# Performance work log

Measured on AMD Instinct MI355X. Metric: run time of the kernel, lower is better.

Reference implementation:

```python
import jax, jax.numpy as jnp
import numpy as np

N, E, NG = 4096, 8192, 256
AF, BF, H, L = 9, 4, 128, 3
LN_EPS = 1e-5


def _layernorm(x, g, b):
    mu = jnp.mean(x, axis=-1, keepdims=True)
    var = jnp.var(x, axis=-1, keepdims=True)
    return (x - mu) * jax.lax.rsqrt(var + LN_EPS) * g + b


def setup_inputs() -> dict:
    key = jax.random.key(0)
    ks = jax.random.split(key, 20)
    x = jax.random.normal(ks[0], (N, AF), dtype=jnp.float32)
    edge_index = jax.random.randint(ks[1], (2, E), 0, N, dtype=jnp.int64)
    edge_attr = jax.random.normal(ks[2], (E, BF), dtype=jnp.float32)
    batch = jnp.sort(jax.random.randint(ks[3], (N,), 0, NG, dtype=jnp.int64))
    s = lambda f: 1.0 / np.sqrt(f)
    return {
        "x": x, "edge_index": edge_index, "edge_attr": edge_attr, "batch": batch,
        "atom_w": jax.random.normal(ks[4], (AF, H), jnp.float32) * s(AF),
        "atom_b": jnp.zeros((H,), jnp.float32),
        # per-layer edge-network params, stacked over L layers
        "e1_w": jax.random.normal(ks[5], (L, BF, H), jnp.float32) * s(BF),
        "e1_b": jnp.zeros((L, H), jnp.float32),
        "e2_w": jax.random.normal(ks[6], (L, H, H * H), jnp.float32) * s(H),
        "e2_b": jnp.zeros((L, H * H), jnp.float32),
        "root_w": jax.random.normal(ks[7], (L, H, H), jnp.float32) * s(H),
        "conv_b": jnp.zeros((L, H), jnp.float32),
        "ln_g": jnp.ones((L, H), jnp.float32),
        "ln_b": jnp.zeros((L, H), jnp.float32),
        "head_w1": jax.random.normal(ks[8], (H, H // 2), jnp.float32) * s(H),
        "head_b1": jnp.zeros((H // 2,), jnp.float32),
        "head_w2": jax.random.normal(ks[9], (H // 2, 1), jnp.float32) * s(H // 2),
        "head_b2": jnp.zeros((1,), jnp.float32),
    }


def reference(x, edge_index, edge_attr, batch, atom_w, atom_b, e1_w, e1_b,
              e2_w, e2_b, root_w, conv_b, ln_g, ln_b, head_w1, head_b1,
              head_w2, head_b2):
    src, dst = edge_index[0], edge_index[1]
    h = jax.nn.relu(x @ atom_w + atom_b)  # [N, H]
    # in-degree for mean aggregation (empty -> 0 via clamp on denominator)
    deg = jax.ops.segment_sum(jnp.ones((E,), h.dtype), dst, num_segments=N)
    denom = jnp.maximum(deg, 1.0)[:, None]
    for l in range(L):
        # edge network: bond features -> per-edge HxH weight matrix
        eh = jax.nn.gelu(edge_attr @ e1_w[l] + e1_b[l], approximate=False)
        w = (eh @ e2_w[l] + e2_b[l]).reshape(E, H, H)  # [E, H, H]
        # gather source node features, per-edge matvec, scatter-mean to dst
        msg = jnp.einsum('ei,eio->eo', h[src], w)  # [E, H]
        agg = jax.ops.segment_sum(msg, dst, num_segments=N) / denom
        h_new = jax.nn.relu(agg + h @ root_w[l] + conv_b[l])
        h = _layernorm(h + h_new, ln_g[l], ln_b[l])
        # dropout: eval mode (identity)
    # global mean pool over graphs
    cnt = jnp.maximum(jax.ops.segment_sum(jnp.ones((N,), h.dtype), batch, num_segments=NG), 1.0)
    mol = jax.ops.segment_sum(h, batch, num_segments=NG) / cnt[:, None]
    hid = jax.nn.gelu(mol @ head_w1 + head_b1, approximate=False)
    logits = (hid @ head_w2 + head_b2).squeeze(-1)  # [NG]
    return logits
```

## Files before the change

### kernel.cpp

```cpp
#include <hip/hip_runtime.h>
#include <hip/hip_bf16.h>

#define N_NODES 4096
#define N_EDGES 8192
#define NGRAPH  256
#define AFEAT   9
#define BFEAT   4
#define H       128
#define NL      3
#define KS      129
#define SPLITS  4
#define TILE_E  64
#define SLICE_SH    16384
#define SLICE_BYTES 32768
#define WREG_BYTES  8192

typedef short short8 __attribute__((ext_vector_type(8)));
typedef short short4v __attribute__((ext_vector_type(4)));
typedef float f32x4 __attribute__((ext_vector_type(4)));

__device__ __forceinline__ short f2b(float f){
    union { float f; unsigned u; } c; c.f = f;
    unsigned r = c.u + 0x7FFFu + ((c.u >> 16) & 1u);
    return (short)(r >> 16);
}
__device__ __forceinline__ float b2f(short b){
    union { unsigned u; float f; } c;
    c.u = ((unsigned)(unsigned short)b) << 16;
    return c.f;
}
__device__ __forceinline__ float gelu_exact(float x){
    return 0.5f * x * (1.0f + erff(x * 0.70710678118654752440f));
}
__device__ __forceinline__ void async_copy16(const void* g, void* l){
    typedef __attribute__((address_space(1))) const char AS1C;
    typedef __attribute__((address_space(3))) char AS3;
    __builtin_amdgcn_global_load_lds((AS1C*)g, (AS3*)l, 16, 0, 0);
}

__global__ void k_prep_b(const float* __restrict__ e2w, const float* __restrict__ e2b,
                         short* __restrict__ bt){
    __shared__ float ts[H][33];
    int b  = blockIdx.x;
    int o0 = (b & 3) * 32;
    int k  = (b >> 2) % KS;
    int l  = (b >> 2) / KS;
    const float* src = (k < H) ? (e2w + ((size_t)l * H + k) * (H * H))
                               : (e2b + (size_t)l * (H * H));
    for (int idx = threadIdx.x; idx < H * 32; idx += 256){
        int i = idx >> 5, op = idx & 31;
        ts[i][op] = src[i * H + o0 + op];
    }
    __syncthreads();
    short* dst = bt + (size_t)(l * KS + k) * SLICE_SH;
    for (int idx = threadIdx.x; idx < 32 * H; idx += 256){
        int j    = idx & 7;
        int quad = (idx >> 3) & 3;
        int op   = (idx >> 5) & 31;
        int ic   = idx >> 10;
        int i    = ic * 32 + quad * 8 + j;
        int o    = o0 + op;
        dst[((((o >> 4) * 4 + ic) * 64) + quad * 16 + (o & 15)) * 8 + j] = f2b(ts[i][op]);
    }
}

__global__ void k_atom(const float* __restrict__ x, const float* __restrict__ aw,
                       const float* __restrict__ ab, float* __restrict__ h,
                       short* __restrict__ hb){
    __shared__ float xs[AFEAT];
    int n = blockIdx.x, o = threadIdx.x;
    if (o < AFEAT) xs[o] = x[n * AFEAT + o];
    __syncthreads();
    float a = ab[o];
    #pragma unroll
    for (int f = 0; f < AFEAT; ++f) a += xs[f] * aw[f * H + o];
    a = fmaxf(a, 0.0f);
    h[(size_t)n * H + o]  = a;
    hb[(size_t)n * H + o] = f2b(a);
}

__global__ void k_deg(const int* __restrict__ ei, int* __restrict__ ideg){
    int e = blockIdx.x * 256 + threadIdx.x;
    if (e < N_EDGES) atomicAdd(&ideg[ei[N_EDGES + e]], 1);
}

__global__ void k_scan(const int* __restrict__ ideg, int* __restrict__ row_ptr,
                       int* __restrict__ cursor){
    __shared__ int part[256];
    int t = threadIdx.x;
    int base = t * 16;
    int loc[16]; int s = 0;
    #pragma unroll
    for (int i = 0; i < 16; ++i){ loc[i] = s; s += ideg[base + i]; }
    part[t] = s;
    __syncthreads();
    if (t == 0){
        int run = 0;
        for (int i = 0; i < 256; ++i){ int v = part[i]; part[i] = run; run += v; }
        row_ptr[N_NODES] = run;
    }
    __syncthreads();
    int off = part[t];
    #pragma unroll
    for (int i = 0; i < 16; ++i){
        row_ptr[base + i] = off + loc[i];
        cursor[base + i]  = off + loc[i];
    }
}

__global__ void k_fill(const int* __restrict__ ei, int* __restrict__ cursor,
                       int* __restrict__ eidx){
    int e = blockIdx.x * 256 + threadIdx.x;
    if (e < N_EDGES){
        int d = ei[N_EDGES + e];
        int pos = atomicAdd(&cursor[d], 1);
        eidx[pos] = e;
    }
}

__global__ void k_edge_mlp(const float* __restrict__ ea, const float* __restrict__ w1,
                           const float* __restrict__ b1, short* __restrict__ ehT){
    __shared__ float as[BFEAT];
    int e = blockIdx.x, o = threadIdx.x;
    if (o < BFEAT) as[o] = ea[e * BFEAT + o];
    __syncthreads();
    #pragma unroll
    for (int l = 0; l < NL; ++l){
        float v = b1[l * H + o];
        #pragma unroll
        for (int f = 0; f < BFEAT; ++f) v += as[f] * w1[(l * BFEAT + f) * H + o];
        v = gelu_exact(v);
        ehT[((size_t)l * KS + o) * N_EDGES + e] = f2b(v);
        if (o == 0) ehT[((size_t)l * KS + H) * N_EDGES + e] = f2b(1.0f);
    }
}

__global__ __launch_bounds__(256, 2)
void k_msg_gemm(const short* __restrict__ bt, const short* __restrict__ ehT,
                const short* __restrict__ hb, const int* __restrict__ ei,
                float* __restrict__ parts, int l){
    __shared__ __align__(16) char smem[2 * 4 * WREG_BYTES + 33 * TILE_E * 2];
    short* ehs = (short*)(smem + 2 * 4 * WREG_BYTES);

    const int tid  = threadIdx.x;
    const int lane = tid & 63, w = tid >> 6;
    const int col  = lane & 15, quad = lane >> 4;

    const int split = blockIdx.x & 3;
    const int tile  = blockIdx.x >> 2;
    const int kbeg  = (KS * split) >> 2;
    const int kend  = (KS * (split + 1)) >> 2;
    const int kcnt  = kend - kbeg;
    const int ebase = tile * TILE_E;

    for (int idx = tid; idx < kcnt * TILE_E; idx += 256){
        int kk = idx >> 6, e = idx & 63;
        ehs[idx] = ehT[((size_t)(l * KS + kbeg + kk)) * N_EDGES + ebase + e];
    }

    short8 gf[4][4];
    #pragma unroll
    for (int m = 0; m < 4; ++m){
        int e = ebase + m * 16 + col;
        int s = ei[e];
        const char* gb = (const char*)hb + ((size_t)s * H + quad * 8) * 2;
        #pragma unroll
        for (int ic = 0; ic < 4; ++ic)
            gf[m][ic] = *(const short8*)(gb + ic * 64);
    }

    float acc[4][2][4];
    #pragma unroll
    for (int m = 0; m < 4; ++m)
        #pragma unroll
        for (int ot = 0; ot < 2; ++ot)
            #pragma unroll
            for (int r = 0; r < 4; ++r) acc[m][ot][r] = 0.0f;

    const char* bsrc = (const char*)bt + (size_t)(l * KS + kbeg) * SLICE_BYTES
                     + w * WREG_BYTES;
    char* lws = smem + w * WREG_BYTES;

    #pragma unroll
    for (int i = 0; i < 8; ++i)
        async_copy16(bsrc + i * 1024 + lane * 16, lws + i * 1024 + lane * 16);

    __syncthreads();

    for (int kk = 0; kk < kcnt; ++kk){
        if (kk + 1 < kcnt){
            const char* g = bsrc + (size_t)(kk + 1) * SLICE_BYTES;
            char* d = lws + ((kk + 1) & 1) * (4 * WREG_BYTES);
            asm volatile("s_waitcnt lgkmcnt(0)" ::: "memory");
            #pragma unroll
            for (int i = 0; i < 8; ++i)
                async_copy16(g + i * 1024 + lane * 16, d + i * 1024 + lane * 16);
            asm volatile("s_waitcnt vmcnt(8)" ::: "memory");
        } else {
            asm volatile("s_waitcnt vmcnt(0)" ::: "memory");
        }
        const char* Bl = lws + (kk & 1) * (4 * WREG_BYTES);

        short4v ev[4];
        #pragma unroll
        for (int m = 0; m < 4; ++m)
            ev[m] = *(const short4v*)(ehs + kk * TILE_E + m * 16 + quad * 4);

        __builtin_amdgcn_s_setprio(1);
        #pragma unroll
        for (int ot = 0; ot < 2; ++ot){
            short8 bf[4];
            #pragma unroll
            for (int ic = 0; ic < 4; ++ic)
                bf[ic] = *(const short8*)(Bl + (ot * 4 + ic) * 1024 + lane * 16);
            #pragma unroll
            for (int m = 0; m < 4; ++m){
                f32x4 U = {0.0f, 0.0f, 0.0f, 0.0f};
                #pragma unroll
                for (int ic = 0; ic < 4; ++ic)
                    U = __builtin_amdgcn_mfma_f32_16x16x32_bf16(gf[m][ic], bf[ic], U, 0, 0, 0);
                #pragma unroll
                for (int r = 0; r < 4; ++r)
                    acc[m][ot][r] += b2f(ev[m][r]) * U[r];
            }
        }
        __builtin_amdgcn_s_setprio(0);
    }

    float* pb = parts + (size_t)split * N_EDGES * H + (size_t)ebase * H + w * 32;
    #pragma unroll
    for (int m = 0; m < 4; ++m)
        #pragma unroll
        for (int r = 0; r < 4; ++r){
            float* row = pb + (m * 16 + quad * 4 + r) * H;
            #pragma unroll
            for (int ot = 0; ot < 2; ++ot)
                row[ot * 16 + col] = acc[m][ot][r];
        }
}

__global__ void k_node(const float* __restrict__ parts, const int* __restrict__ eidx,
                       const int* __restrict__ row_ptr,
                       const float* __restrict__ rw, const float* __restrict__ cb,
                       const float* __restrict__ lg, const float* __restrict__ lb,
                       float* __restrict__ h, short* __restrict__ hb, int l){
    __shared__ float hs[H];
    __shared__ float rsum[2], rsq[2];
    int n = blockIdx.x, o = threadIdx.x;
    float hv = h[(size_t)n * H + o];
    hs[o] = hv;
    int p0 = row_ptr[n], p1 = row_ptr[n + 1];
    float a = 0.0f;
    for (int p = p0; p < p1; ++p){
        const float* pr = parts + (size_t)eidx[p] * H + o;
        #pragma unroll
        for (int s = 0; s < SPLITS; ++s) a += pr[(size_t)s * N_EDGES * H];
    }
    int d = p1 - p0;
    a *= 1.0f / (float)(d > 0 ? d : 1);
    __syncthreads();
    float root = cb[l * H + o];
    const float* W = rw + (size_t)l * H * H;
    #pragma unroll 8
    for (int i = 0; i < H; ++i) root += hs[i] * W[i * H + o];
    float hn = fmaxf(a + root, 0.0f);
    float v  = hv + hn;
    float s = v, q = v * v;
    #pragma unroll
    for (int off = 32; off > 0; off >>= 1){
        s += __shfl_down(s, off, 64);
        q += __shfl_down(q, off, 64);
    }
    if ((o & 63) == 0){ rsum[o >> 6] = s; rsq[o >> 6] = q; }
    __syncthreads();
    float S = rsum[0] + rsum[1], Q = rsq[0] + rsq[1];
    float mean = S * (1.0f / H);
    float var  = Q * (1.0f / H) - mean * mean;
    float out  = (v - mean) * rsqrtf(var + 1e-5f) * lg[l * H + o] + lb[l * H + o];
    h[(size_t)n * H + o]  = out;
    hb[(size_t)n * H + o] = f2b(out);
}

__global__ void k_pool(const float* __restrict__ h, const int* __restrict__ batch,
                       float* __restrict__ molsum, float* __restrict__ cnt){
    int idx = blockIdx.x * 256 + threadIdx.x;
    int n = idx >> 7, o = idx & 127;
    int b = batch[n];
    atomicAdd(&molsum[b * H + o], h[idx]);
    if (o == 0) atomicAdd(&cnt[b], 1.0f);
}

__global__ void k_head(const float* __restrict__ molsum, const float* __restrict__ cnt,
                       const float* __restrict__ w1, const float* __restrict__ b1,
                       const float* __restrict__ w2, const float* __restrict__ b2,
                       float* __restrict__ out){
    __shared__ float mol[H];
    int g = blockIdx.x, t = threadIdx.x;
    float c = fmaxf(cnt[g], 1.0f);
    mol[t]      = molsum[g * H + t] / c;
    mol[t + 64] = molsum[g * H + t + 64] / c;
    __syncthreads();
    float a = b1[t];
    #pragma unroll 8
    for (int i = 0; i < H; ++i) a += mol[i] * w1[i * 64 + t];
    float hid = gelu_exact(a);
    float p = hid * w2[t];
    #pragma unroll
    for (int off = 32; off > 0; off >>= 1) p += __shfl_down(p, off, 64);
    if (t == 0) out[g] = p + b2[0];
}

extern "C" void kernel_launch(void* const* d_in, const int* in_sizes, int n_in,
                              void* d_out, int out_size, void* d_ws, size_t ws_size,
                              hipStream_t stream){
    (void)in_sizes; (void)n_in; (void)out_size; (void)ws_size;
    const float* x     = (const float*)d_in[0];
    const int*   ei    = (const int*)  d_in[1];
    const float* ea    = (const float*)d_in[2];
    const int*   batch = (const int*)  d_in[3];
    const float* aw    = (const float*)d_in[4];
    const float* ab    = (const float*)d_in[5];
    const float* e1w   = (const float*)d_in[6];
    const float* e1b   = (const float*)d_in[7];
    const float* e2w   = (const float*)d_in[8];
    const float* e2b   = (const float*)d_in[9];
    const float* rw    = (const float*)d_in[10];
    const float* cb    = (const float*)d_in[11];
    const float* lg    = (const float*)d_in[12];
    const float* lb    = (const float*)d_in[13];
    const float* hw1   = (const float*)d_in[14];
    const float* hb1   = (const float*)d_in[15];
    const float* hw2   = (const float*)d_in[16];
    const float* hb2   = (const float*)d_in[17];
    float* out = (float*)d_out;

    char* p = (char*)d_ws;
    auto carve = [&](size_t bytes){ char* r = p; p += (bytes + 255) & ~(size_t)255; return r; };
    short* bt     = (short*)carve((size_t)NL * KS * SLICE_SH * 2);
    float* h      = (float*)carve((size_t)N_NODES * H * 4);
    short* hbuf   = (short*)carve((size_t)N_NODES * H * 2);
    short* ehT    = (short*)carve((size_t)NL * KS * N_EDGES * 2);
    float* parts  = (float*)carve((size_t)SPLITS * N_EDGES * H * 4);
    int*   ideg   = (int*)  carve((size_t)N_NODES * 4);
    int*   row_ptr= (int*)  carve((size_t)(N_NODES + 1) * 4);
    int*   cursor = (int*)  carve((size_t)N_NODES * 4);
    int*   eidx   = (int*)  carve((size_t)N_EDGES * 4);
    float* molsum = (float*)carve((size_t)NGRAPH * H * 4);
    float* cnt    = (float*)carve((size_t)NGRAPH * 4);

    hipMemsetAsync(ideg, 0, (size_t)N_NODES * 4, stream);
    hipMemsetAsync(molsum, 0, (size_t)NGRAPH * H * 4, stream);
    hipMemsetAsync(cnt, 0, (size_t)NGRAPH * 4, stream);

    k_prep_b<<<NL * KS * 4, 256, 0, stream>>>(e2w, e2b, bt);
    k_atom<<<N_NODES, H, 0, stream>>>(x, aw, ab, h, hbuf);
    k_deg<<<N_EDGES / 256, 256, 0, stream>>>(ei, ideg);
    k_scan<<<1, 256, 0, stream>>>(ideg, row_ptr, cursor);
    k_fill<<<N_EDGES / 256, 256, 0, stream>>>(ei, cursor, eidx);
    k_edge_mlp<<<N_EDGES, H, 0, stream>>>(ea, e1w, e1b, ehT);

    for (int l = 0; l < NL; ++l){
        k_msg_gemm<<<(N_EDGES / TILE_E) * SPLITS, 256, 0, stream>>>(bt, ehT, hbuf, ei, parts, l);
        k_node<<<N_NODES, H, 0, stream>>>(parts, eidx, row_ptr, rw, cb, lg, lb, h, hbuf, l);
    }
    k_pool<<<N_NODES * H / 256, 256, 0, stream>>>(h, batch, molsum, cnt);
    k_head<<<NGRAPH, 64, 0, stream>>>(molsum, cnt, hw1, hb1, hw2, hb2, out);
}
```

Before: 320.1 us.

## Load message-GEMM B slices straight to registers and split output columns across blocks

Drops the async global-to-LDS double buffer for the per-edge weight slices. Each wave now loads its B fragments straight into registers with a two-slice ping-pong prefetch. The output columns are split into two halves across twice as many blocks, so each wave computes 16 columns instead of 32, which cuts register and LDS pressure and raises parallelism. The edge-MLP activations are stored as fp32 instead of bf16, removing the bf16 conversion in the inner loop. In exchange, the hidden-feature gather and ehT loads are repeated per half, and the ehT buffer is twice as large.

```diff
diff --git a/kernel.cpp b/kernel.cpp
--- a/kernel.cpp
+++ b/kernel.cpp
@@ -13,10 +13,8 @@
 #define TILE_E  64
 #define SLICE_SH    16384
 #define SLICE_BYTES 32768
-#define WREG_BYTES  8192
 
 typedef short short8 __attribute__((ext_vector_type(8)));
-typedef short short4v __attribute__((ext_vector_type(4)));
 typedef float f32x4 __attribute__((ext_vector_type(4)));
 
 __device__ __forceinline__ short f2b(float f){
@@ -24,18 +22,8 @@
     unsigned r = c.u + 0x7FFFu + ((c.u >> 16) & 1u);
     return (short)(r >> 16);
 }
-__device__ __forceinline__ float b2f(short b){
-    union { unsigned u; float f; } c;
-    c.u = ((unsigned)(unsigned short)b) << 16;
-    return c.f;
-}
 __device__ __forceinline__ float gelu_exact(float x){
     return 0.5f * x * (1.0f + erff(x * 0.70710678118654752440f));
-}
-__device__ __forceinline__ void async_copy16(const void* g, void* l){
-    typedef __attribute__((address_space(1))) const char AS1C;
-    typedef __attribute__((address_space(3))) char AS3;
-    __builtin_amdgcn_global_load_lds((AS1C*)g, (AS3*)l, 16, 0, 0);
 }
 
 __global__ void k_prep_b(const float* __restrict__ e2w, const float* __restrict__ e2b,
@@ -119,7 +107,7 @@
 }
 
 __global__ void k_edge_mlp(const float* __restrict__ ea, const float* __restrict__ w1,
-                           const float* __restrict__ b1, short* __restrict__ ehT){
+                           const float* __restrict__ b1, float* __restrict__ ehT){
     __shared__ float as[BFEAT];
     int e = blockIdx.x, o = threadIdx.x;
     if (o < BFEAT) as[o] = ea[e * BFEAT + o];
@@ -130,24 +118,25 @@
         #pragma unroll
         for (int f = 0; f < BFEAT; ++f) v += as[f] * w1[(l * BFEAT + f) * H + o];
         v = gelu_exact(v);
-        ehT[((size_t)l * KS + o) * N_EDGES + e] = f2b(v);
-        if (o == 0) ehT[((size_t)l * KS + H) * N_EDGES + e] = f2b(1.0f);
+        ehT[((size_t)l * KS + o) * N_EDGES + e] = v;
+        if (o == 0) ehT[((size_t)l * KS + H) * N_EDGES + e] = 1.0f;
     }
 }
 
 __global__ __launch_bounds__(256, 2)
-void k_msg_gemm(const short* __restrict__ bt, const short* __restrict__ ehT,
+void k_msg_gemm(const short* __restrict__ bt, const float* __restrict__ ehT,
                 const short* __restrict__ hb, const int* __restrict__ ei,
                 float* __restrict__ parts, int l){
-    __shared__ __align__(16) char smem[2 * 4 * WREG_BYTES + 33 * TILE_E * 2];
-    short* ehs = (short*)(smem + 2 * 4 * WREG_BYTES);
+    __shared__ __align__(16) float ehs[33 * TILE_E];
 
     const int tid  = threadIdx.x;
     const int lane = tid & 63, w = tid >> 6;
     const int col  = lane & 15, quad = lane >> 4;
 
     const int split = blockIdx.x & 3;
-    const int tile  = blockIdx.x >> 2;
+    const int ohalf = (blockIdx.x >> 2) & 1;
+    const int tile  = blockIdx.x >> 3;
+    const int t     = ohalf * 4 + w;
     const int kbeg  = (KS * split) >> 2;
     const int kend  = (KS * (split + 1)) >> 2;
     const int kcnt  = kend - kbeg;
@@ -169,74 +158,57 @@
             gf[m][ic] = *(const short8*)(gb + ic * 64);
     }
 
-    float acc[4][2][4];
+    float acc[4][4];
     #pragma unroll
     for (int m = 0; m < 4; ++m)
         #pragma unroll
-        for (int ot = 0; ot < 2; ++ot)
-            #pragma unroll
-            for (int r = 0; r < 4; ++r) acc[m][ot][r] = 0.0f;
+        for (int r = 0; r < 4; ++r) acc[m][r] = 0.0f;
 
     const char* bsrc = (const char*)bt + (size_t)(l * KS + kbeg) * SLICE_BYTES
-                     + w * WREG_BYTES;
-    char* lws = smem + w * WREG_BYTES;
-
-    #pragma unroll
-    for (int i = 0; i < 8; ++i)
-        async_copy16(bsrc + i * 1024 + lane * 16, lws + i * 1024 + lane * 16);
-
-    __syncthreads();
-
-    for (int kk = 0; kk < kcnt; ++kk){
-        if (kk + 1 < kcnt){
-            const char* g = bsrc + (size_t)(kk + 1) * SLICE_BYTES;
-            char* d = lws + ((kk + 1) & 1) * (4 * WREG_BYTES);
-            asm volatile("s_waitcnt lgkmcnt(0)" ::: "memory");
-            #pragma unroll
-            for (int i = 0; i < 8; ++i)
-                async_copy16(g + i * 1024 + lane * 16, d + i * 1024 + lane * 16);
-            asm volatile("s_waitcnt vmcnt(8)" ::: "memory");
-        } else {
-            asm volatile("s_waitcnt vmcnt(0)" ::: "memory");
-        }
-        const char* Bl = lws + (kk & 1) * (4 * WREG_BYTES);
-
-        short4v ev[4];
-        #pragma unroll
-        for (int m = 0; m < 4; ++m)
-            ev[m] = *(const short4v*)(ehs + kk * TILE_E + m * 16 + quad * 4);
-
+                     + t * 4096 + lane * 16;
+
+    short8 X[4], Y[4];
+
+    auto loadB = [&](short8 (&B)[4], int kk){
+        const char* p = bsrc + (size_t)kk * SLICE_BYTES;
+        #pragma unroll
+        for (int ic = 0; ic < 4; ++ic)
+            B[ic] = *(const short8*)(p + ic * 1024);
+    };
+    auto computeB = [&](const short8 (&B)[4], int kk){
         __builtin_amdgcn_s_setprio(1);
         #pragma unroll
-        for (int ot = 0; ot < 2; ++ot){
-            short8 bf[4];
+        for (int m = 0; m < 4; ++m){
+            f32x4 ev = *(const f32x4*)(ehs + kk * TILE_E + m * 16 + quad * 4);
+            f32x4 U = {0.0f, 0.0f, 0.0f, 0.0f};
             #pragma unroll
             for (int ic = 0; ic < 4; ++ic)
-                bf[ic] = *(const short8*)(Bl + (ot * 4 + ic) * 1024 + lane * 16);
+                U = __builtin_amdgcn_mfma_f32_16x16x32_bf16(gf[m][ic], B[ic], U, 0, 0, 0);
             #pragma unroll
-            for (int m = 0; m < 4; ++m){
-                f32x4 U = {0.0f, 0.0f, 0.0f, 0.0f};
-                #pragma unroll
-                for (int ic = 0; ic < 4; ++ic)
-                    U = __builtin_amdgcn_mfma_f32_16x16x32_bf16(gf[m][ic], bf[ic], U, 0, 0, 0);
-                #pragma unroll
-                for (int r = 0; r < 4; ++r)
-                    acc[m][ot][r] += b2f(ev[m][r]) * U[r];
-            }
+            for (int r = 0; r < 4; ++r)
+                acc[m][r] += ev[r] * U[r];
         }
         __builtin_amdgcn_s_setprio(0);
-    }
-
-    float* pb = parts + (size_t)split * N_EDGES * H + (size_t)ebase * H + w * 32;
+    };
+
+    loadB(X, 0);
+    __syncthreads();
+
+    int kk = 0;
+    for (; kk + 2 <= kcnt; kk += 2){
+        loadB(Y, kk + 1);
+        computeB(X, kk);
+        if (kk + 2 < kcnt) loadB(X, kk + 2);
+        computeB(Y, kk + 1);
+    }
+    if (kk < kcnt) computeB(X, kk);
+
+    float* pb = parts + (size_t)split * N_EDGES * H + (size_t)ebase * H + t * 16;
     #pragma unroll
     for (int m = 0; m < 4; ++m)
         #pragma unroll
-        for (int r = 0; r < 4; ++r){
-            float* row = pb + (m * 16 + quad * 4 + r) * H;
-            #pragma unroll
-            for (int ot = 0; ot < 2; ++ot)
-                row[ot * 16 + col] = acc[m][ot][r];
-        }
+        for (int r = 0; r < 4; ++r)
+            pb[(size_t)(m * 16 + quad * 4 + r) * H + col] = acc[m][r];
 }
 
 __global__ void k_node(const float* __restrict__ parts, const int* __restrict__ eidx,
@@ -339,7 +311,7 @@
     short* bt     = (short*)carve((size_t)NL * KS * SLICE_SH * 2);
     float* h      = (float*)carve((size_t)N_NODES * H * 4);
     short* hbuf   = (short*)carve((size_t)N_NODES * H * 2);
-    short* ehT    = (short*)carve((size_t)NL * KS * N_EDGES * 2);
+    float* ehT    = (float*)carve((size_t)NL * KS * N_EDGES * 4);
     float* parts  = (float*)carve((size_t)SPLITS * N_EDGES * H * 4);
     int*   ideg   = (int*)  carve((size_t)N_NODES * 4);
     int*   row_ptr= (int*)  carve((size_t)(N_NODES + 1) * 4);
@@ -360,7 +332,7 @@
     k_edge_mlp<<<N_EDGES, H, 0, stream>>>(ea, e1w, e1b, ehT);
 
     for (int l = 0; l < NL; ++l){
-        k_msg_gemm<<<(N_EDGES / TILE_E) * SPLITS, 256, 0, stream>>>(bt, ehT, hbuf, ei, parts, l);
+        k_msg_gemm<<<(N_EDGES / TILE_E) * 2 * SPLITS, 256, 0, stream>>>(bt, ehT, hbuf, ei, parts, l);
         k_node<<<N_NODES, H, 0, stream>>>(parts, eidx, row_ptr, rw, cb, lg, lb, h, hbuf, l);
     }
     k_pool<<<N_NODES * H / 256, 256, 0, stream>>>(h, batch, molsum, cnt);
```

New measurement: 320.5 us. Within noise of the previous version (+0.1%).
